# Performance work log

Measured on AMD Instinct MI355X. Metric: run time of the kernel, lower is better.

Reference implementation:

```python
import jax, jax.numpy as jnp
import numpy as np

DIM = 256
NUM_HEADS = 8
HEAD_DIM = DIM // NUM_HEADS


def rope_sincos(H, W, head_dim, dtype=jnp.float32):
    n = head_dim // 4
    angle = 1.0 / (10000.0 ** jnp.linspace(0.0, 1.0, n))
    angle = jnp.repeat(angle, 2)  # (head_dim//2,)
    ph = jnp.arange(H, dtype=dtype)[:, None] * angle[None, :]  # (H, d/2)
    pw = jnp.arange(W, dtype=dtype)[:, None] * angle[None, :]  # (W, d/2)
    sin_h = jnp.broadcast_to(jnp.sin(ph)[:, None, :], (H, W, 2 * n))
    sin_w = jnp.broadcast_to(jnp.sin(pw)[None, :, :], (H, W, 2 * n))
    cos_h = jnp.broadcast_to(jnp.cos(ph)[:, None, :], (H, W, 2 * n))
    cos_w = jnp.broadcast_to(jnp.cos(pw)[None, :, :], (H, W, 2 * n))
    sin = jnp.concatenate([sin_h, sin_w], -1).reshape(H * W, head_dim)
    cos = jnp.concatenate([cos_h, cos_w], -1).reshape(H * W, head_dim)
    return sin, cos


def rotate_every_two(x):
    x1 = x[..., 0::2]
    x2 = x[..., 1::2]
    return jnp.stack([-x2, x1], axis=-1).reshape(x.shape)


def theta_shift(x, sin, cos):
    return x * cos + rotate_every_two(x) * sin


def conv1x1(x, w, b):
    # x: (B,C,H,W), w: (O,C,1,1)
    return jnp.einsum('bchw,oc->bohw', x, w[:, :, 0, 0]) + b[None, :, None, None]


def depthwise5x5(x, w, b):
    # x: (B,C,H,W), w: (C,1,5,5), groups=C
    y = jax.lax.conv_general_dilated(
        x, w, window_strides=(1, 1), padding=((2, 2), (2, 2)),
        feature_group_count=x.shape[1],
        dimension_numbers=('NCHW', 'OIHW', 'NCHW'))
    return y + b[None, :, None, None]


def setup_inputs() -> dict:
    key = jax.random.key(0)
    ks = jax.random.split(key, 7)
    B, C, H, W = 8, DIM, 64, 64
    x = jax.random.normal(ks[0], (B, C, H, W), dtype=jnp.float32)
    qkvo_w = 0.02 * jax.random.normal(ks[1], (4 * C, C, 1, 1), dtype=jnp.float32)
    qkvo_b = jnp.zeros((4 * C,), dtype=jnp.float32)
    lepe_w = 0.02 * jax.random.normal(ks[2], (C, 1, 5, 5), dtype=jnp.float32)
    lepe_b = jnp.zeros((C,), dtype=jnp.float32)
    proj_w = 0.02 * jax.random.normal(ks[3], (C, C, 1, 1), dtype=jnp.float32)
    proj_b = jnp.zeros((C,), dtype=jnp.float32)
    return {'x': x, 'qkvo_w': qkvo_w, 'qkvo_b': qkvo_b,
            'lepe_w': lepe_w, 'lepe_b': lepe_b,
            'proj_w': proj_w, 'proj_b': proj_b}


def reference(x, qkvo_w, qkvo_b, lepe_w, lepe_b, proj_w, proj_b):
    B, C, H, W = x.shape
    n, d = NUM_HEADS, HEAD_DIM
    L = H * W
    scale = d ** (-0.5)

    sin, cos = rope_sincos(H, W, d, dtype=x.dtype)  # (L, d)

    qkvo = conv1x1(x, qkvo_w, qkvo_b)          # (B, 4C, H, W)
    qkv = qkvo[:, :3 * C]                       # (B, 3C, H, W)
    o = qkvo[:, 3 * C:]                         # (B, C, H, W)
    lepe = depthwise5x5(qkv[:, 2 * C:], lepe_w, lepe_b)  # (B, C, H, W)

    # 'b (m n d) h w -> m b n (h w) d'
    qkv_r = qkv.reshape(B, 3, n, d, H * W).transpose(1, 0, 2, 4, 3)  # (3,B,n,L,d)
    q, k, v = qkv_r[0], qkv_r[1], qkv_r[2]

    q = jax.nn.elu(q) + 1.0
    k = jax.nn.elu(k) + 1.0

    kmean = k.mean(axis=2, keepdims=True)               # (B,n,1,d)
    z = jnp.einsum('bnld,bnmd->bnlm', q, kmean) * scale  # (B,n,L,1)

    q = theta_shift(q, sin, cos)
    k = theta_shift(k, sin, cos)

    c = (scale / L) ** 0.5
    kv = jnp.einsum('bnld,bnle->bnde', k * c, v * c)     # (B,n,d,d)
    vmean = v.mean(axis=2, keepdims=True)                # (B,n,1,d)

    res = jnp.einsum('bnld,bnde->bnle', q, kv) * (1.0 + 1.0 / (z + 1e-6)) - z * vmean
    # 'b n (h w) d -> b (n d) h w'
    res = res.reshape(B, n, H, W, d).transpose(0, 1, 4, 2, 3).reshape(B, C, H, W)
    res = res + lepe
    return conv1x1(res * o, proj_w, proj_b)
```

## Files before the change

kernel.cpp:

```cpp
#include <hip/hip_runtime.h>
#include <math.h>

typedef unsigned short u16;
typedef unsigned int u32;
typedef unsigned long long u64;
typedef __attribute__((ext_vector_type(8))) short short8;
typedef __attribute__((ext_vector_type(4))) float f32x4;
typedef __attribute__((ext_vector_type(16))) float f32x16;

static constexpr float SCALE = 0.17677669529663687f;
static constexpr float C2    = 0.17677669529663687f / 4096.f;

__device__ __forceinline__ float bf2f(u16 u){
  union { u32 i; float f; } v; v.i = ((u32)u) << 16; return v.f;
}
__device__ __forceinline__ u16 f2bf(float f){
  union { float fl; u32 i; } v; v.fl = f;
  u32 r = v.i + 0x7fffu + ((v.i >> 16) & 1u);
  return (u16)(r >> 16);
}
__device__ __forceinline__ float eluP(float x){ return x > 0.f ? x + 1.f : __expf(x); }
__device__ __forceinline__ float rfreq(int j){
  const float t[8] = {1.f, 0.2682695795f, 0.0719685673f, 0.0193069773f,
                      0.0051794747f, 0.0013894955f, 0.0003727594f, 1e-4f};
  return t[j];
}
__device__ __forceinline__ void gload16(const u16* g, u16* l){
  __builtin_amdgcn_global_load_lds(
      (const __attribute__((address_space(1))) u32*)g,
      (__attribute__((address_space(3))) u32*)l, 16, 0, 0);
}

__global__ __launch_bounds__(256) void k_pre(
    const float* __restrict__ x, const float* __restrict__ qw, const float* __restrict__ pw,
    u16* __restrict__ XT, u16* __restrict__ Whi, u16* __restrict__ Wlo,
    u16* __restrict__ Phi, u16* __restrict__ Plo, float* __restrict__ KM0,
    float* __restrict__ SCS)
{
  if (blockIdx.z < 8){
    __shared__ float t[64][65];
    int l0 = blockIdx.x * 64, c0 = blockIdx.y * 64, b = blockIdx.z;
    const float* xp = x + (((long)b * 256 + c0) << 12) + l0;
    #pragma unroll
    for (int rep = 0; rep < 4; rep++){
      int idx = threadIdx.x + rep * 256;
      int r = idx >> 4, ch = (idx & 15) * 4;
      float4 f = *(const float4*)&xp[((long)r << 12) + ch];
      t[r][ch] = f.x; t[r][ch+1] = f.y; t[r][ch+2] = f.z; t[r][ch+3] = f.w;
    }
    __syncthreads();
    int r2 = threadIdx.x >> 2, c8 = (threadIdx.x & 3) * 16;
    u32 w[8];
    #pragma unroll
    for (int j = 0; j < 8; j++){
      float v0 = t[c8 + 2*j][r2], v1 = t[c8 + 2*j + 1][r2];
      w[j] = (u32)f2bf(v0) | ((u32)f2bf(v1) << 16);
    }
    long ob = (((long)b << 12) << 8) + ((long)(l0 + r2) << 8) + c0 + c8;
    *(uint4*)&XT[ob]     = make_uint4(w[0], w[1], w[2], w[3]);
    *(uint4*)&XT[ob + 8] = make_uint4(w[4], w[5], w[6], w[7]);
  } else {
    int bid = (blockIdx.z - 8) * 256 + blockIdx.y * 64 + blockIdx.x;
    int idx = bid * 256 + threadIdx.x;
    if (idx < 262144){
      float v = qw[idx]; u16 h = f2bf(v);
      Whi[idx] = h; Wlo[idx] = f2bf(v - bf2f(h));
    }
    if (idx < 65536){
      float v = pw[idx]; u16 h = f2bf(v);
      Phi[idx] = h; Plo[idx] = f2bf(v - bf2f(h));
    }
    if (bid == 0){
      #pragma unroll
      for (int i = 0; i < 16; i++) KM0[threadIdx.x + i * 256] = 0.f;
    }
    if (bid == 1){
      #pragma unroll
      for (int r = 0; r < 2; r++){
        int t2 = threadIdx.x + r * 256;
        int jj = t2 >> 6, pp = t2 & 63;
        float sn, cs; sincosf(rfreq(jj) * (float)pp, &sn, &cs);
        SCS[t2] = sn; SCS[512 + t2] = cs;
      }
    }
  }
}

__global__ __launch_bounds__(256) void k_gemmA(
    const u16* __restrict__ Whi_, const u16* __restrict__ Wlo_,
    const u16* __restrict__ Bh_,
    const float* __restrict__ bias, const float* __restrict__ SCS_,
    u16* __restrict__ Q16, u16* __restrict__ K16,
    u16* __restrict__ V16, u16* __restrict__ O16,
    float* __restrict__ KMb, float* __restrict__ VMb, int mtoff)
{
  __shared__ __align__(16) u16 AhS[2][4096];
  __shared__ __align__(16) u16 AlS[2][4096];
  __shared__ __align__(16) u16 BhS[2][4096];
  __shared__ float scs[2][8][64];
  const int tid = threadIdx.x;
  const int nt = blockIdx.x, mt = mtoff + blockIdx.y, b = blockIdx.z;
  const int m0 = mt * 128, n0 = nt * 128;
  const int wave = tid >> 6, lane = tid & 63;
  const int wm = wave & 1, wn = wave >> 1, qu = lane >> 4, ln = lane & 15;
  const int range = m0 >> 8;

  const u16* bhp = Bh_ + (((long)b << 12) << 8);

  const int l4 = lane >> 2, c4 = lane & 3;
  const int gch = (c4 ^ ((l4 >> 1) & 3)) * 8;
  const int fch = (qu ^ ((ln >> 1) & 3)) * 8;

  auto stage = [&](int buf, int kk){
    #pragma unroll
    for (int t = 0; t < 2; t++){
      int rw = wave * 32 + t * 16;
      int ga = (m0 + rw + l4) * 256 + kk + gch;
      long gb = (long)(n0 + rw + l4) * 256 + kk + gch;
      gload16(&Whi_[ga], &AhS[buf][rw * 32]);
      gload16(&Wlo_[ga], &AlS[buf][rw * 32]);
      gload16(&bhp[gb],  &BhS[buf][rw * 32]);
    }
  };

  f32x4 acc[4][4];
  #pragma unroll
  for (int im = 0; im < 4; im++)
    #pragma unroll
    for (int in = 0; in < 4; in++)
      #pragma unroll
      for (int r = 0; r < 4; r++) acc[im][in][r] = 0.f;

  stage(0, 0);
  if (range == 1){
    #pragma unroll
    for (int r = 0; r < 4; r++){
      int idx = tid + r * 256;
      ((float*)scs)[idx] = SCS_[idx];
    }
  }
  __syncthreads();

  int cur = 0;
  #pragma unroll
  for (int ks = 0; ks < 8; ks++){
    if (ks < 7) stage(cur ^ 1, (ks + 1) * 32);
    const u16* Ah = AhS[cur];
    const u16* Al = AlS[cur];
    const u16* Bc = BhS[cur];
    short8 fbh[4];
    #pragma unroll
    for (int in = 0; in < 4; in++){
      int row = wn * 64 + in * 16 + ln;
      fbh[in] = *(const short8*)&Bc[row * 32 + fch];
    }
    #pragma unroll
    for (int im = 0; im < 4; im++){
      int row = wm * 64 + im * 16 + ln;
      short8 fah = *(const short8*)&Ah[row * 32 + fch];
      short8 fal = *(const short8*)&Al[row * 32 + fch];
      #pragma unroll
      for (int in = 0; in < 4; in++){
        acc[im][in] = __builtin_amdgcn_mfma_f32_16x16x32_bf16(fah, fbh[in], acc[im][in], 0, 0, 0);
        acc[im][in] = __builtin_amdgcn_mfma_f32_16x16x32_bf16(fal, fbh[in], acc[im][in], 0, 0, 0);
      }
    }
    if (ks < 7) __syncthreads();
    cur ^= 1;
  }

  u16* dst = (range == 0) ? Q16 : (range == 1) ? K16 : (range == 2) ? V16 : O16;
  #pragma unroll
  for (int im = 0; im < 4; im++){
    const int mb = m0 + wm * 64 + im * 16 + qu * 4;
    float v[4][4];
    #pragma unroll
    for (int r = 0; r < 4; r++){
      float bia = bias[mb + r];
      #pragma unroll
      for (int in = 0; in < 4; in++){
        float t = acc[im][in][r] + bia;
        v[r][in] = (range < 2) ? eluP(t) : t;
      }
    }
    if (range == 1 || range == 2){
      float* mbuf = (range == 1) ? KMb : VMb;
      #pragma unroll
      for (int r = 0; r < 4; r++){
        float s = v[r][0] + v[r][1] + v[r][2] + v[r][3];
        s += __shfl_xor(s, 1); s += __shfl_xor(s, 2);
        s += __shfl_xor(s, 4); s += __shfl_xor(s, 8);
        if (ln == 0) atomicAdd(&mbuf[b * 256 + ((mb + r) & 255)], s);
      }
    }
    if (range == 1){
      const int p0 = (mb & 31) >> 1;
      #pragma unroll
      for (int half = 0; half < 2; half++){
        int p = p0 + half, j = p & 7;
        #pragma unroll
        for (int in = 0; in < 4; in++){
          int n = n0 + wn * 64 + in * 16 + ln;
          int pos = (p < 8) ? (n >> 6) : (n & 63);
          float sn = scs[0][j][pos], cs = scs[1][j][pos];
          float a = v[2*half][in], bb = v[2*half+1][in];
          v[2*half][in]   = a * cs - bb * sn;
          v[2*half+1][in] = bb * cs + a * sn;
        }
      }
    }
    #pragma unroll
    for (int r = 0; r < 4; r++){
      u16* rowp = dst + (((long)b * 256 + ((mb + r) & 255)) << 12);
      #pragma unroll
      for (int in = 0; in < 4; in++){
        int n = n0 + wn * 64 + in * 16 + ln;
        rowp[n] = f2bf(v[r][in]);
      }
    }
  }
}

__global__ __launch_bounds__(256) void k_mid(
    const u16* __restrict__ K16, const u16* __restrict__ V16,
    const float* __restrict__ lw, const float* __restrict__ lb,
    u16* __restrict__ Tb16, float* __restrict__ KVb)
{
  if (blockIdx.y >= 2){
    __shared__ float tile[20][68];
    int ht = blockIdx.x, ch = blockIdx.y - 2, b = blockIdx.z;
    int h0 = ht * 16;
    const u16* vp = V16 + (((long)b * 256 + ch) << 12);
    const float* __restrict__ wlp = lw + ch * 25;
    for (int idx = threadIdx.x; idx < 20 * 68; idx += 256){
      int r = idx / 68, c = idx % 68;
      int gh = h0 + r - 2, gw = c - 2;
      float v = 0.f;
      if (gh >= 0 && gh < 64 && gw >= 0 && gw < 64) v = bf2f(vp[(gh << 6) + gw]);
      tile[r][c] = v;
    }
    __syncthreads();
    const float bia = lb[ch];
    #pragma unroll
    for (int r2 = 0; r2 < 4; r2++){
      int idx = threadIdx.x + r2 * 256;
      int oh = idx >> 6, ow = idx & 63;
      float s = bia;
      #pragma unroll
      for (int i = 0; i < 5; i++)
        #pragma unroll
        for (int j = 0; j < 5; j++) s += tile[oh + i][ow + j] * wlp[i * 5 + j];
      Tb16[(((long)b * 256 + ch) << 12) + ((h0 + oh) << 6) + ow] = f2bf(s);
    }
  } else {
    __shared__ float red[4][1024];
    int kvIdx = blockIdx.y * 32 + blockIdx.z * 4 + blockIdx.x;
    int n = kvIdx & 7, b = kvIdx >> 3;
    const int tid = threadIdx.x, wave = tid >> 6, lane = tid & 63;
    const u16* kp = K16 + (((long)(b * 256 + n * 32)) << 12);
    const u16* vp = V16 + (((long)(b * 256 + n * 32)) << 12);
    const int m = lane & 31, kh = lane >> 5;
    const long row = ((long)m << 12);

    f32x16 acc;
    #pragma unroll
    for (int r = 0; r < 16; r++) acc[r] = 0.f;
    #pragma unroll 4
    for (int it = 0; it < 64; it++){
      int l = wave * 1024 + it * 16 + kh * 8;
      short8 a  = *(const short8*)&kp[row + l];
      short8 bf = *(const short8*)&vp[row + l];
      acc = __builtin_amdgcn_mfma_f32_32x32x16_bf16(a, bf, acc, 0, 0, 0);
    }
    #pragma unroll
    for (int reg = 0; reg < 16; reg++){
      int rr = (reg & 3) + 8 * (reg >> 2) + 4 * kh;
      red[wave][rr * 32 + m] = acc[reg];
    }
    __syncthreads();
    #pragma unroll
    for (int i = tid; i < 1024; i += 256){
      float s = red[0][i] + red[1][i] + red[2][i] + red[3][i];
      KVb[(((long)b * 8 + n) << 10) + i] = s * C2;
    }
  }
}

__global__ __launch_bounds__(128) void k_res(
    const u16* __restrict__ Q16, const float* __restrict__ KMb,
    const float* __restrict__ KVb, const float* __restrict__ VMb,
    const u16* __restrict__ O16, const u16* __restrict__ Tb16,
    const float* __restrict__ SCS_, u16* __restrict__ TT16)
{
  __shared__ float scs[2][8][64];
  __shared__ __align__(16) u64 tts[128 * 9];
  const int b = blockIdx.z, n = blockIdx.y, tid = threadIdx.x;
  #pragma unroll
  for (int r = 0; r < 8; r++){
    int idx = tid + r * 128;
    ((float*)scs)[idx] = SCS_[idx];
  }
  __syncthreads();

  const float* __restrict__ kv  = KVb + (((long)b * 8 + n) << 10);
  const float* __restrict__ kmp = KMb + b * 256 + n * 32;
  const float* __restrict__ vmp = VMb + b * 256 + n * 32;

  const int l0 = blockIdx.x * 128;
  const int l = l0 + tid;
  const long cbase = ((long)(b * 256 + n * 32)) << 12;

  float q[32];
  #pragma unroll
  for (int d = 0; d < 32; d++) q[d] = bf2f(Q16[cbase + ((long)d << 12) + l]);
  float z = 0.f;
  #pragma unroll
  for (int d = 0; d < 32; d++) z += q[d] * kmp[d];
  z *= SCALE * (1.f / 4096.f);
  #pragma unroll
  for (int p = 0; p < 16; p++){
    int pos = (p < 8) ? (l >> 6) : (l & 63);
    float sn = scs[0][p & 7][pos], cs = scs[1][p & 7][pos];
    float q0 = q[2*p], q1 = q[2*p+1];
    q[2*p]   = q0 * cs - q1 * sn;
    q[2*p+1] = q1 * cs + q0 * sn;
  }

  float acc[32];
  #pragma unroll
  for (int e = 0; e < 32; e++) acc[e] = 0.f;
  #pragma unroll 8
  for (int d = 0; d < 32; d++){
    float qd = q[d];
    #pragma unroll
    for (int ec = 0; ec < 8; ec++){
      float4 kvv = *(const float4*)&kv[d * 32 + ec * 4];
      acc[ec*4+0] += qd * kvv.x;
      acc[ec*4+1] += qd * kvv.y;
      acc[ec*4+2] += qd * kvv.z;
      acc[ec*4+3] += qd * kvv.w;
    }
  }

  const float f = 1.f + 1.f / (z + 1e-6f);
  const float zv = z * (1.f / 4096.f);
  u32 w[16];
  #pragma unroll
  for (int e = 0; e < 32; e++){
    long off = cbase + ((long)e << 12) + l;
    float val = (acc[e] * f - zv * vmp[e] + bf2f(Tb16[off])) * bf2f(O16[off]);
    u16 h = f2bf(val);
    if (e & 1) w[e >> 1] |= ((u32)h << 16);
    else       w[e >> 1] = h;
  }
  #pragma unroll
  for (int j = 0; j < 8; j++)
    tts[tid * 9 + j] = (u64)w[2*j] | ((u64)w[2*j+1] << 32);
  __syncthreads();
  #pragma unroll
  for (int it = 0; it < 4; it++){
    int row = (tid >> 2) + 32 * it;
    int cc = tid & 3;
    u64 a  = tts[row * 9 + cc * 2];
    u64 bb = tts[row * 9 + cc * 2 + 1];
    long orow = (((long)b << 12) << 8) + ((long)(l0 + row) << 8) + n * 32 + cc * 8;
    *(uint4*)&TT16[orow] = make_uint4((u32)a, (u32)(a >> 32), (u32)bb, (u32)(bb >> 32));
  }
}

__global__ __launch_bounds__(256) void k_gemmP(
    const u16* __restrict__ Phi_, const u16* __restrict__ Plo_,
    const u16* __restrict__ TT16, const float* __restrict__ bias,
    float* __restrict__ out)
{
  __shared__ __align__(16) u16 AhS[3][4096];
  __shared__ __align__(16) u16 AlS[3][4096];
  __shared__ __align__(16) u16 BhS[3][4096];
  const int tid = threadIdx.x;
  const int nt = blockIdx.x, mt = blockIdx.y, b = blockIdx.z;
  const int m0 = mt * 128, n0 = nt * 128;
  const int wave = tid >> 6, lane = tid & 63;
  const int wm = wave & 1, wn = wave >> 1, qu = lane >> 4, ln = lane & 15;

  const u16* bhp = TT16 + (((long)b << 12) << 8);
  const int l4 = lane >> 2, c4 = lane & 3;
  const int gch = (c4 ^ ((l4 >> 1) & 3)) * 8;
  const int fch = (qu ^ ((ln >> 1) & 3)) * 8;

  auto stage = [&](int buf, int kk){
    #pragma unroll
    for (int t = 0; t < 2; t++){
      int rw = wave * 32 + t * 16;
      int ga = (m0 + rw + l4) * 256 + kk + gch;
      long gb = (long)(n0 + rw + l4) * 256 + kk + gch;
      gload16(&Phi_[ga], &AhS[buf][rw * 32]);
      gload16(&Plo_[ga], &AlS[buf][rw * 32]);
      gload16(&bhp[gb],  &BhS[buf][rw * 32]);
    }
  };

  f32x4 acc[4][4];
  #pragma unroll
  for (int im = 0; im < 4; im++)
    #pragma unroll
    for (int in = 0; in < 4; in++)
      #pragma unroll
      for (int r = 0; r < 4; r++) acc[im][in][r] = 0.f;

  stage(0, 0);
  stage(1, 32);

  #pragma unroll
  for (int ks = 0; ks < 8; ks++){
    if (ks < 7) asm volatile("s_waitcnt vmcnt(6)" ::: "memory");
    else        asm volatile("s_waitcnt vmcnt(0)" ::: "memory");
    __builtin_amdgcn_s_barrier();
    __builtin_amdgcn_sched_barrier(0);
    if (ks < 6) stage((ks + 2) % 3, (ks + 2) * 32);
    const u16* Ah = AhS[ks % 3];
    const u16* Al = AlS[ks % 3];
    const u16* Bc = BhS[ks % 3];
    short8 fbh[4];
    #pragma unroll
    for (int in = 0; in < 4; in++){
      int row = wn * 64 + in * 16 + ln;
      fbh[in] = *(const short8*)&Bc[row * 32 + fch];
    }
    #pragma unroll
    for (int im = 0; im < 4; im++){
      int row = wm * 64 + im * 16 + ln;
      short8 fah = *(const short8*)&Ah[row * 32 + fch];
      short8 fal = *(const short8*)&Al[row * 32 + fch];
      #pragma unroll
      for (int in = 0; in < 4; in++){
        acc[im][in] = __builtin_amdgcn_mfma_f32_16x16x32_bf16(fah, fbh[in], acc[im][in], 0, 0, 0);
        acc[im][in] = __builtin_amdgcn_mfma_f32_16x16x32_bf16(fal, fbh[in], acc[im][in], 0, 0, 0);
      }
    }
  }

  #pragma unroll
  for (int im = 0; im < 4; im++){
    int mbase = m0 + wm * 64 + im * 16 + qu * 4;
    #pragma unroll
    for (int r = 0; r < 4; r++){
      int m = mbase + r;
      float bia = bias[m];
      float* row = out + (((long)b * 256 + m) << 12);
      #pragma unroll
      for (int in = 0; in < 4; in++){
        int n = n0 + wn * 64 + in * 16 + ln;
        row[n] = acc[im][in][r] + bia;
      }
    }
  }
}

extern "C" void kernel_launch(void* const* d_in, const int* in_sizes, int n_in,
                              void* d_out, int out_size, void* d_ws, size_t ws_size,
                              hipStream_t stream)
{
  const float* x  = (const float*)d_in[0];
  const float* qw = (const float*)d_in[1];
  const float* qb = (const float*)d_in[2];
  const float* lw = (const float*)d_in[3];
  const float* lb = (const float*)d_in[4];
  const float* pw = (const float*)d_in[5];
  const float* pb = (const float*)d_in[6];

  u16* W    = (u16*)d_ws;
  u16* Q16  = W;
  u16* K16  = Q16 + 8388608;
  u16* V16  = K16 + 8388608;
  u16* O16  = V16 + 8388608;
  u16* Tb16 = O16 + 8388608;
  u16* XT   = Tb16 + 8388608;
  u16* Whi  = XT + 8388608;
  u16* Wlo  = Whi + 262144;
  u16* Phi  = Wlo + 262144;
  u16* Plo  = Phi + 65536;
  float* KMb = (float*)(Plo + 65536);
  float* VMb = KMb + 2048;
  float* KVb = VMb + 2048;
  float* SCS = KVb + 65536;
  size_t total_bytes = (6ull*8388608 + 2*262144 + 2*65536) * 2 + (2048+2048+65536+1024) * 4;
  if (ws_size < total_bytes) return;

  u16* TT16 = XT;

  k_pre<<<dim3(64, 4, 12), 256, 0, stream>>>(x, qw, pw, XT, Whi, Wlo, Phi, Plo, KMb, SCS);
  k_gemmA<<<dim3(32, 4, 8), 256, 0, stream>>>(Whi, Wlo, XT, qb, SCS,
                                              Q16, K16, V16, O16, KMb, VMb, 0);
  k_gemmA<<<dim3(32, 4, 8), 256, 0, stream>>>(Whi, Wlo, XT, qb, SCS,
                                              Q16, K16, V16, O16, KMb, VMb, 4);
  k_mid<<<dim3(4, 258, 8), 256, 0, stream>>>(K16, V16, lw, lb, Tb16, KVb);
  k_res<<<dim3(32, 8, 8), 128, 0, stream>>>(Q16, KMb, KVb, VMb, O16, Tb16, SCS, TT16);
  k_gemmP<<<dim3(32, 2, 8), 256, 0, stream>>>(Phi, Plo, TT16, pb, (float*)d_out);
}
```

Before: 235.6 us.

## Merge gemmA launches, split KV reduction over L with atomics, register-block depthwise conv

New measurement: 209.5 us. 1.12x faster.

```diff
diff --git a/kernel.cpp b/kernel.cpp
--- a/kernel.cpp
+++ b/kernel.cpp
@@ -35,7 +35,7 @@
     const float* __restrict__ x, const float* __restrict__ qw, const float* __restrict__ pw,
     u16* __restrict__ XT, u16* __restrict__ Whi, u16* __restrict__ Wlo,
     u16* __restrict__ Phi, u16* __restrict__ Plo, float* __restrict__ KM0,
-    float* __restrict__ SCS)
+    float* __restrict__ SCS, float* __restrict__ KVb)
 {
   if (blockIdx.z < 8){
     __shared__ float t[64][65];
@@ -83,6 +83,11 @@
         SCS[t2] = sn; SCS[512 + t2] = cs;
       }
     }
+    if (bid >= 2 && bid < 10){
+      int base = (bid - 2) * 8192 + threadIdx.x;
+      #pragma unroll
+      for (int i = 0; i < 32; i++) KVb[base + i * 256] = 0.f;
+    }
   }
 }
 
@@ -92,14 +97,14 @@
     const float* __restrict__ bias, const float* __restrict__ SCS_,
     u16* __restrict__ Q16, u16* __restrict__ K16,
     u16* __restrict__ V16, u16* __restrict__ O16,
-    float* __restrict__ KMb, float* __restrict__ VMb, int mtoff)
+    float* __restrict__ KMb, float* __restrict__ VMb)
 {
   __shared__ __align__(16) u16 AhS[2][4096];
   __shared__ __align__(16) u16 AlS[2][4096];
   __shared__ __align__(16) u16 BhS[2][4096];
   __shared__ float scs[2][8][64];
   const int tid = threadIdx.x;
-  const int nt = blockIdx.x, mt = mtoff + blockIdx.y, b = blockIdx.z;
+  const int nt = blockIdx.x, mt = blockIdx.y, b = blockIdx.z;
   const int m0 = mt * 128, n0 = nt * 128;
   const int wave = tid >> 6, lane = tid & 63;
   const int wm = wave & 1, wn = wave >> 1, qu = lane >> 4, ln = lane & 15;
@@ -226,9 +231,9 @@
     const float* __restrict__ lw, const float* __restrict__ lb,
     u16* __restrict__ Tb16, float* __restrict__ KVb)
 {
-  if (blockIdx.y >= 2){
+  if (blockIdx.y >= 8){
     __shared__ float tile[20][68];
-    int ht = blockIdx.x, ch = blockIdx.y - 2, b = blockIdx.z;
+    int ht = blockIdx.x, ch = blockIdx.y - 8, b = blockIdx.z;
     int h0 = ht * 16;
     const u16* vp = V16 + (((long)b * 256 + ch) << 12);
     const float* __restrict__ wlp = lw + ch * 25;
@@ -241,33 +246,43 @@
     }
     __syncthreads();
     const float bia = lb[ch];
-    #pragma unroll
-    for (int r2 = 0; r2 < 4; r2++){
-      int idx = threadIdx.x + r2 * 256;
-      int oh = idx >> 6, ow = idx & 63;
-      float s = bia;
-      #pragma unroll
-      for (int i = 0; i < 5; i++)
-        #pragma unroll
-        for (int j = 0; j < 5; j++) s += tile[oh + i][ow + j] * wlp[i * 5 + j];
-      Tb16[(((long)b * 256 + ch) << 12) + ((h0 + oh) << 6) + ow] = f2bf(s);
-    }
+    const int ow = threadIdx.x & 63, oh0 = (threadIdx.x >> 6) * 4;
+    float s0 = bia, s1 = bia, s2 = bia, s3 = bia;
+    #pragma unroll
+    for (int j = 0; j < 5; j++){
+      float c0 = tile[oh0+0][ow+j], c1 = tile[oh0+1][ow+j];
+      float c2 = tile[oh0+2][ow+j], c3 = tile[oh0+3][ow+j];
+      float c4 = tile[oh0+4][ow+j], c5 = tile[oh0+5][ow+j];
+      float c6 = tile[oh0+6][ow+j], c7 = tile[oh0+7][ow+j];
+      float w0 = wlp[j], w1 = wlp[5+j], w2 = wlp[10+j], w3 = wlp[15+j], w4 = wlp[20+j];
+      s0 += c0*w0 + c1*w1 + c2*w2 + c3*w3 + c4*w4;
+      s1 += c1*w0 + c2*w1 + c3*w2 + c4*w3 + c5*w4;
+      s2 += c2*w0 + c3*w1 + c4*w2 + c5*w3 + c6*w4;
+      s3 += c3*w0 + c4*w1 + c5*w2 + c6*w3 + c7*w4;
+    }
+    u16* tp = Tb16 + (((long)b * 256 + ch) << 12) + ((h0 + oh0) << 6) + ow;
+    tp[0]   = f2bf(s0);
+    tp[64]  = f2bf(s1);
+    tp[128] = f2bf(s2);
+    tp[192] = f2bf(s3);
   } else {
     __shared__ float red[4][1024];
     int kvIdx = blockIdx.y * 32 + blockIdx.z * 4 + blockIdx.x;
-    int n = kvIdx & 7, b = kvIdx >> 3;
+    int seg = kvIdx >> 6, rem = kvIdx & 63;
+    int n = rem & 7, b = rem >> 3;
     const int tid = threadIdx.x, wave = tid >> 6, lane = tid & 63;
     const u16* kp = K16 + (((long)(b * 256 + n * 32)) << 12);
     const u16* vp = V16 + (((long)(b * 256 + n * 32)) << 12);
     const int m = lane & 31, kh = lane >> 5;
     const long row = ((long)m << 12);
+    const int lbase = seg * 1024 + wave * 256;
 
     f32x16 acc;
     #pragma unroll
     for (int r = 0; r < 16; r++) acc[r] = 0.f;
     #pragma unroll 4
-    for (int it = 0; it < 64; it++){
-      int l = wave * 1024 + it * 16 + kh * 8;
+    for (int it = 0; it < 16; it++){
+      int l = lbase + it * 16 + kh * 8;
       short8 a  = *(const short8*)&kp[row + l];
       short8 bf = *(const short8*)&vp[row + l];
       acc = __builtin_amdgcn_mfma_f32_32x32x16_bf16(a, bf, acc, 0, 0, 0);
@@ -281,23 +296,23 @@
     #pragma unroll
     for (int i = tid; i < 1024; i += 256){
       float s = red[0][i] + red[1][i] + red[2][i] + red[3][i];
-      KVb[(((long)b * 8 + n) << 10) + i] = s * C2;
-    }
-  }
-}
-
-__global__ __launch_bounds__(128) void k_res(
+      atomicAdd(&KVb[(((long)b * 8 + n) << 10) + i], s * C2);
+    }
+  }
+}
+
+__global__ __launch_bounds__(256) void k_res(
     const u16* __restrict__ Q16, const float* __restrict__ KMb,
     const float* __restrict__ KVb, const float* __restrict__ VMb,
     const u16* __restrict__ O16, const u16* __restrict__ Tb16,
     const float* __restrict__ SCS_, u16* __restrict__ TT16)
 {
   __shared__ float scs[2][8][64];
-  __shared__ __align__(16) u64 tts[128 * 9];
+  __shared__ __align__(16) u64 tts[256 * 9];
   const int b = blockIdx.z, n = blockIdx.y, tid = threadIdx.x;
   #pragma unroll
-  for (int r = 0; r < 8; r++){
-    int idx = tid + r * 128;
+  for (int r = 0; r < 4; r++){
+    int idx = tid + r * 256;
     ((float*)scs)[idx] = SCS_[idx];
   }
   __syncthreads();
@@ -306,7 +321,7 @@
   const float* __restrict__ kmp = KMb + b * 256 + n * 32;
   const float* __restrict__ vmp = VMb + b * 256 + n * 32;
 
-  const int l0 = blockIdx.x * 128;
+  const int l0 = blockIdx.x * 256;
   const int l = l0 + tid;
   const long cbase = ((long)(b * 256 + n * 32)) << 12;
 
@@ -359,7 +374,7 @@
   __syncthreads();
   #pragma unroll
   for (int it = 0; it < 4; it++){
-    int row = (tid >> 2) + 32 * it;
+    int row = (tid >> 2) + 64 * it;
     int cc = tid & 3;
     u64 a  = tts[row * 9 + cc * 2];
     u64 bb = tts[row * 9 + cc * 2 + 1];
@@ -488,12 +503,10 @@
 
   u16* TT16 = XT;
 
-  k_pre<<<dim3(64, 4, 12), 256, 0, stream>>>(x, qw, pw, XT, Whi, Wlo, Phi, Plo, KMb, SCS);
-  k_gemmA<<<dim3(32, 4, 8), 256, 0, stream>>>(Whi, Wlo, XT, qb, SCS,
-                                              Q16, K16, V16, O16, KMb, VMb, 0);
-  k_gemmA<<<dim3(32, 4, 8), 256, 0, stream>>>(Whi, Wlo, XT, qb, SCS,
-                                              Q16, K16, V16, O16, KMb, VMb, 4);
-  k_mid<<<dim3(4, 258, 8), 256, 0, stream>>>(K16, V16, lw, lb, Tb16, KVb);
-  k_res<<<dim3(32, 8, 8), 128, 0, stream>>>(Q16, KMb, KVb, VMb, O16, Tb16, SCS, TT16);
+  k_pre<<<dim3(64, 4, 12), 256, 0, stream>>>(x, qw, pw, XT, Whi, Wlo, Phi, Plo, KMb, SCS, KVb);
+  k_gemmA<<<dim3(32, 8, 8), 256, 0, stream>>>(Whi, Wlo, XT, qb, SCS,
+                                              Q16, K16, V16, O16, KMb, VMb);
+  k_mid<<<dim3(4, 264, 8), 256, 0, stream>>>(K16, V16, lw, lb, Tb16, KVb);
+  k_res<<<dim3(16, 8, 8), 256, 0, stream>>>(Q16, KMb, KVb, VMb, O16, Tb16, SCS, TT16);
   k_gemmP<<<dim3(32, 2, 8), 256, 0, stream>>>(Phi, Plo, TT16, pb, (float*)d_out);
 }
```
